# Optimization experiments

Hardware: AMD Instinct MI355X
Metric: run time of the kernel (lower is better)

The kernel has to match this reference:

```python
import jax, jax.numpy as jnp
import numpy as np

PROX_TOL = 5
SEG_PENALTY = 3.0
SEG_REWARD = 0.3
CLASS_WEIGHTS = np.array([0.1, 5.0, 5.0], dtype=np.float32)


def setup_inputs() -> dict:
    key = jax.random.key(0)
    k1, k2, k3 = jax.random.split(key, 3)
    B, S, C = 256, 16384, 3
    logits = jax.random.normal(k1, (B, S, C), dtype=jnp.float32)
    labels = jax.random.randint(k2, (B, S), 0, 3, dtype=jnp.int64)
    tokens = jax.random.randint(k3, (B, S), 0, 1000, dtype=jnp.int64)
    return {"logits": logits, "labels": labels, "tokens": tokens}


def _window_any(mask, tol):
    # sliding 'any' over [t-tol, t+tol], clipped at sequence edges ('SAME' padding)
    m = mask.astype(jnp.float32)
    r = jax.lax.reduce_window(m, 0.0, jax.lax.max, (1, 2 * tol + 1), (1, 1), 'SAME')
    return r > 0.0


def reference(logits, labels, tokens):
    B, S, C = logits.shape
    cw = jnp.asarray(CLASS_WEIGHTS, dtype=logits.dtype)

    # weighted cross-entropy, reduction='none' -> w[y] * nll  [B, S]
    logp = jax.nn.log_softmax(logits, axis=-1)
    nll = -jnp.take_along_axis(logp, labels[..., None], axis=-1)[..., 0]
    base_loss = nll * cw[labels]

    predictions = jnp.argmax(logits, axis=-1)
    pred_switch = predictions >= 1   # [B, S]
    true_switch = labels >= 1        # [B, S]

    # segmentation adjustment (tokens is not None): for predicted switches,
    # the t+1 < S check overwrites the penalty with the reward, so:
    #   t <  S-1        -> reward
    #   t == S-1, t>=1  -> penalty (offset loop fired)
    pos = jnp.arange(S)
    adj = jnp.where(pred_switch & (pos < S - 1), SEG_REWARD,
                    jnp.where(pred_switch & (pos == S - 1) & (pos >= 1), SEG_PENALTY, 1.0))
    base_loss = base_loss * adj.astype(base_loss.dtype)

    # proximity reward: true switch with any predicted switch within +/- tol -> *0.1
    pred_near = _window_any(pred_switch, PROX_TOL)
    base_loss = jnp.where(true_switch & pred_near, base_loss * 0.1, base_loss)

    # false-positive penalty: predicted switch farther than tol from every true
    # switch -> *2.0 (only applied if the sequence has at least one true switch)
    true_near = _window_any(true_switch, PROX_TOL)
    has_true = jnp.any(true_switch, axis=1, keepdims=True)
    base_loss = jnp.where(pred_switch & has_true & (~true_near), base_loss * 2.0, base_loss)

    valid_mask = (labels != -100).astype(base_loss.dtype)
    return (base_loss * valid_mask).sum() / valid_mask.sum()
```

## Files before the change

kernel.cpp:

```cpp
#include <hip/hip_runtime.h>

#define SEQ 16384
#define TOL 5
#define CHUNK 1024
#define NCHUNK (SEQ / CHUNK)
#define NW (CHUNK / 64)
#define JITER (CHUNK / 256)
#define NROW 256
#define NBLK (NROW * NCHUNK)
#define TOTAL_VALID 4194304.0


__global__ __launch_bounds__(256, 4) void switch_loss_kernel(
    const float* __restrict__ logits,
    const int* __restrict__ labels,
    float* __restrict__ blk_sum, float* __restrict__ blk_fp,
    int* __restrict__ blk_any)
{
    const int row = blockIdx.y;
    const int chunk = blockIdx.x;
    const int s0 = chunk * CHUNK;
    const int t = threadIdx.x;
    const int w = t >> 6;
    const int lane = t & 63;

    __shared__ unsigned long long ps[NW + 2];
    __shared__ unsigned long long ts[NW + 2];
    __shared__ float wsum[4], wfp[4];
    __shared__ int wany[4];

    const float* __restrict__ lrow = logits + (size_t)row * (SEQ * 3);
    const int* __restrict__ labrow = labels + (size_t)row * SEQ;

    float l0v[JITER], l1v[JITER], l2v[JITER];
    int yv[JITER];
    #pragma unroll
    for (int j = 0; j < JITER; ++j) {
        const int s = s0 + j * 256 + t;
        l0v[j] = lrow[s * 3 + 0];
        l1v[j] = lrow[s * 3 + 1];
        l2v[j] = lrow[s * 3 + 2];
        yv[j]  = labrow[s];
    }

    if (w == 0) {
        const int pos = s0 - 64 + lane;
        const bool act = (lane >= 64 - TOL) && (pos >= 0);
        bool psw = false, tsw = false;
        if (act) {
            const float h0 = lrow[pos * 3 + 0];
            const float h1 = lrow[pos * 3 + 1];
            const float h2 = lrow[pos * 3 + 2];
            psw = (h1 > h0) || (h2 > fmaxf(h0, h1));
            const int y = labrow[pos];
            tsw = (y >= 1) && (y <= 2);
        }
        const unsigned long long bp = __ballot(psw);
        const unsigned long long bt = __ballot(tsw);
        if (lane == 0) { ps[0] = bp; ts[0] = bt; }
    } else if (w == 1) {
        const int pos = s0 + CHUNK + lane;
        const bool act = (lane < TOL) && (pos < SEQ);
        bool psw = false, tsw = false;
        if (act) {
            const float h0 = lrow[pos * 3 + 0];
            const float h1 = lrow[pos * 3 + 1];
            const float h2 = lrow[pos * 3 + 2];
            psw = (h1 > h0) || (h2 > fmaxf(h0, h1));
            const int y = labrow[pos];
            tsw = (y >= 1) && (y <= 2);
        }
        const unsigned long long bp = __ballot(psw);
        const unsigned long long bt = __ballot(tsw);
        if (lane == 0) { ps[NW + 1] = bp; ts[NW + 1] = bt; }
    }

    float lossv[JITER];
    unsigned pswbits = 0, tswbits = 0;
    unsigned long long my_ts_or = 0ull;

    #pragma unroll
    for (int j = 0; j < JITER; ++j) {
        const int s = s0 + j * 256 + t;
        const float l0 = l0v[j], l1 = l1v[j], l2 = l2v[j];
        const int y = yv[j];

        const float m01 = fmaxf(l0, l1);
        const float m = fmaxf(m01, l2);
        const bool psw = (l1 > l0) || (l2 > m01);

        const float sum = __expf(l0 - m) + __expf(l1 - m) + __expf(l2 - m);
        const float lse = m + __logf(sum);

        const bool valid = (y >= 0) && (y <= 2);
        const bool tsw = valid && (y >= 1);
        const float ly = (y == 0) ? l0 : ((y == 1) ? l1 : l2);
        const float wgt = (y == 0) ? 0.1f : 5.0f;
        float loss = valid ? (lse - ly) * wgt : 0.0f;

        const float adj = psw ? ((s < SEQ - 1) ? 0.3f : 3.0f) : 1.0f;
        lossv[j] = loss * adj;

        pswbits |= (unsigned)psw << j;
        tswbits |= (unsigned)tsw << j;

        const unsigned long long bp = __ballot(psw);
        const unsigned long long bt = __ballot(tsw);
        my_ts_or |= bt;
        if (lane == 0) { ps[1 + j * 4 + w] = bp; ts[1 + j * 4 + w] = bt; }
    }
    if (lane == 0) wany[w] = (my_ts_or != 0ull) ? 1 : 0;
    __syncthreads();

    float lsum = 0.0f, lfp = 0.0f;

    #pragma unroll
    for (int j = 0; j < JITER; ++j) {
        const int s = s0 + j * 256 + t;
        const bool psw = (pswbits >> j) & 1u;
        const bool tsw = (tswbits >> j) & 1u;

        int lo = s - TOL; lo = (lo < 0) ? 0 : lo;
        int hi = s + TOL; hi = (hi > SEQ - 1) ? (SEQ - 1) : hi;
        const int len = hi - lo + 1;
        const int rel = lo - s0 + 64;
        const int qq = rel >> 6;
        const int sh = rel & 63;

        unsigned long long pw = ps[qq] >> sh;
        unsigned long long tw = ts[qq] >> sh;
        if (sh + len > 64) {
            pw |= ps[qq + 1] << (64 - sh);
            tw |= ts[qq + 1] << (64 - sh);
        }
        const unsigned long long mlen = (1ull << len) - 1ull;
        const bool pred_near = (pw & mlen) != 0ull;
        const bool true_near = (tw & mlen) != 0ull;

        float loss = lossv[j];
        if (tsw && pred_near) loss *= 0.1f;
        lsum += loss;
        if (psw && !true_near) lfp += loss;
    }

    #pragma unroll
    for (int off = 32; off > 0; off >>= 1) {
        lsum += __shfl_down(lsum, off, 64);
        lfp  += __shfl_down(lfp, off, 64);
    }
    if (lane == 0) { wsum[w] = lsum; wfp[w] = lfp; }
    __syncthreads();
    if (t == 0) {
        const int slot = row * NCHUNK + chunk;
        blk_sum[slot] = wsum[0] + wsum[1] + wsum[2] + wsum[3];
        blk_fp[slot]  = wfp[0] + wfp[1] + wfp[2] + wfp[3];
        blk_any[slot] = wany[0] | wany[1] | wany[2] | wany[3];
    }
}

__global__ void finalize_kernel(const float* __restrict__ blk_sum,
                                const float* __restrict__ blk_fp,
                                const int* __restrict__ blk_any,
                                float* __restrict__ out) {
    const int t = threadIdx.x;
    const int w = t >> 6, lane = t & 63;
    __shared__ double wsum[4];

    float s = 0.0f, f = 0.0f;
    int any = 0;
    #pragma unroll
    for (int c = 0; c < NCHUNK; ++c) {
        const int slot = t * NCHUNK + c;
        s += blk_sum[slot];
        f += blk_fp[slot];
        any |= blk_any[slot];
    }
    double v = (double)s + (any ? (double)f : 0.0);
    #pragma unroll
    for (int off = 32; off > 0; off >>= 1)
        v += __shfl_down(v, off, 64);
    if (lane == 0) wsum[w] = v;
    __syncthreads();
    if (t == 0)
        out[0] = (float)((wsum[0] + wsum[1] + wsum[2] + wsum[3]) / TOTAL_VALID);
}

extern "C" void kernel_launch(void* const* d_in, const int* in_sizes, int n_in,
                              void* d_out, int out_size, void* d_ws, size_t ws_size,
                              hipStream_t stream) {
    const float* logits = (const float*)d_in[0];
    const int* labels = (const int*)d_in[1];
    (void)in_sizes; (void)n_in; (void)out_size; (void)ws_size;

    float* blk_sum = (float*)d_ws;
    float* blk_fp = blk_sum + NBLK;
    int* blk_any = (int*)(blk_fp + NBLK);
    float* out = (float*)d_out;

    switch_loss_kernel<<<dim3(NCHUNK, NROW), 256, 0, stream>>>(
        logits, labels, blk_sum, blk_fp, blk_any);
    finalize_kernel<<<1, 256, 0, stream>>>(blk_sum, blk_fp, blk_any, out);
}
```

Measured before the change: 108.4 us.

## Vectorize logits/label loads with contiguous per-thread positions and nibble-packed bitmasks

Each thread now owns four consecutive positions and loads its 12 logits and 4 labels as 128-bit non-temporal vector loads instead of strided scalar loads. Because a thread's positions are no longer spread one per wave slot, the predicted and true switch bitmasks are rebuilt by writing per-thread nibbles to shared memory and having 32 threads assemble the 64-bit words. This targets load instruction count and coalescing on a memory-bound kernel. The cost is an extra shared-memory pass and one more barrier.

```diff
diff --git a/kernel.cpp b/kernel.cpp
--- a/kernel.cpp
+++ b/kernel.cpp
@@ -5,10 +5,13 @@
 #define CHUNK 1024
 #define NCHUNK (SEQ / CHUNK)
 #define NW (CHUNK / 64)
-#define JITER (CHUNK / 256)
+#define PPT 4
 #define NROW 256
 #define NBLK (NROW * NCHUNK)
 #define TOTAL_VALID 4194304.0
+
+typedef float f32x4 __attribute__((ext_vector_type(4)));
+typedef int i32x4 __attribute__((ext_vector_type(4)));
 
 
 __global__ __launch_bounds__(256, 4) void switch_loss_kernel(
@@ -26,22 +29,26 @@
 
     __shared__ unsigned long long ps[NW + 2];
     __shared__ unsigned long long ts[NW + 2];
+    __shared__ unsigned char nib[256];
     __shared__ float wsum[4], wfp[4];
     __shared__ int wany[4];
 
     const float* __restrict__ lrow = logits + (size_t)row * (SEQ * 3);
     const int* __restrict__ labrow = labels + (size_t)row * SEQ;
 
-    float l0v[JITER], l1v[JITER], l2v[JITER];
-    int yv[JITER];
-    #pragma unroll
-    for (int j = 0; j < JITER; ++j) {
-        const int s = s0 + j * 256 + t;
-        l0v[j] = lrow[s * 3 + 0];
-        l1v[j] = lrow[s * 3 + 1];
-        l2v[j] = lrow[s * 3 + 2];
-        yv[j]  = labrow[s];
-    }
+    const f32x4* __restrict__ lrow4 = (const f32x4*)(lrow + (size_t)s0 * 3);
+    const f32x4 fa = __builtin_nontemporal_load(&lrow4[3 * t + 0]);
+    const f32x4 fb = __builtin_nontemporal_load(&lrow4[3 * t + 1]);
+    const f32x4 fc = __builtin_nontemporal_load(&lrow4[3 * t + 2]);
+    const i32x4 lab = __builtin_nontemporal_load(&((const i32x4*)(labrow + s0))[t]);
+
+    float L0[PPT], L1[PPT], L2[PPT];
+    int yv[PPT];
+    L0[0] = fa.x; L1[0] = fa.y; L2[0] = fa.z;
+    L0[1] = fa.w; L1[1] = fb.x; L2[1] = fb.y;
+    L0[2] = fb.z; L1[2] = fb.w; L2[2] = fc.x;
+    L0[3] = fc.y; L1[3] = fc.z; L2[3] = fc.w;
+    yv[0] = lab.x; yv[1] = lab.y; yv[2] = lab.z; yv[3] = lab.w;
 
     if (w == 0) {
         const int pos = s0 - 64 + lane;
@@ -75,19 +82,18 @@
         if (lane == 0) { ps[NW + 1] = bp; ts[NW + 1] = bt; }
     }
 
-    float lossv[JITER];
-    unsigned pswbits = 0, tswbits = 0;
-    unsigned long long my_ts_or = 0ull;
-
-    #pragma unroll
-    for (int j = 0; j < JITER; ++j) {
-        const int s = s0 + j * 256 + t;
-        const float l0 = l0v[j], l1 = l1v[j], l2 = l2v[j];
+    float lossv[PPT];
+    unsigned pn = 0, tn = 0;
+
+    #pragma unroll
+    for (int j = 0; j < PPT; ++j) {
+        const int s = s0 + 4 * t + j;
+        const float l0 = L0[j], l1 = L1[j], l2 = L2[j];
         const int y = yv[j];
 
         const float m01 = fmaxf(l0, l1);
+        const bool psw = (l1 > l0) || (l2 > m01);
         const float m = fmaxf(m01, l2);
-        const bool psw = (l1 > l0) || (l2 > m01);
 
         const float sum = __expf(l0 - m) + __expf(l1 - m) + __expf(l2 - m);
         const float lse = m + __logf(sum);
@@ -101,24 +107,37 @@
         const float adj = psw ? ((s < SEQ - 1) ? 0.3f : 3.0f) : 1.0f;
         lossv[j] = loss * adj;
 
-        pswbits |= (unsigned)psw << j;
-        tswbits |= (unsigned)tsw << j;
-
-        const unsigned long long bp = __ballot(psw);
-        const unsigned long long bt = __ballot(tsw);
-        my_ts_or |= bt;
-        if (lane == 0) { ps[1 + j * 4 + w] = bp; ts[1 + j * 4 + w] = bt; }
-    }
-    if (lane == 0) wany[w] = (my_ts_or != 0ull) ? 1 : 0;
+        pn |= (unsigned)psw << j;
+        tn |= (unsigned)tsw << j;
+    }
+    nib[t] = (unsigned char)(pn | (tn << 4));
+    {
+        const unsigned long long anyb = __ballot(tn != 0);
+        if (lane == 0) wany[w] = (anyb != 0ull) ? 1 : 0;
+    }
+    __syncthreads();
+
+    if (t < 32) {
+        const int wi = t & 15;
+        const bool isTs = (t >= 16);
+        unsigned long long word = 0ull;
+        #pragma unroll
+        for (int i = 0; i < 16; ++i) {
+            const unsigned b = nib[wi * 16 + i];
+            const unsigned bits = isTs ? (b >> 4) : (b & 0xFu);
+            word |= (unsigned long long)bits << (4 * i);
+        }
+        if (isTs) ts[1 + wi] = word; else ps[1 + wi] = word;
+    }
     __syncthreads();
 
     float lsum = 0.0f, lfp = 0.0f;
 
     #pragma unroll
-    for (int j = 0; j < JITER; ++j) {
-        const int s = s0 + j * 256 + t;
-        const bool psw = (pswbits >> j) & 1u;
-        const bool tsw = (tswbits >> j) & 1u;
+    for (int j = 0; j < PPT; ++j) {
+        const int s = s0 + 4 * t + j;
+        const bool psw = (pn >> j) & 1u;
+        const bool tsw = (tn >> j) & 1u;
 
         int lo = s - TOL; lo = (lo < 0) ? 0 : lo;
         int hi = s + TOL; hi = (hi > SEQ - 1) ? (SEQ - 1) : hi;
```

New measurement: 117.7 us. 1.09x slower.
